# Optimization experiments

Hardware: AMD Instinct MI355X
Metric: run time of the kernel (lower is better)

## Reference

```python
import jax, jax.numpy as jnp
import numpy as np

L_F, D_F = 32, 16      # fast window / hop
L_S, D_S = 32, 16      # slow window / hop
H = 32                 # SSM hidden dim
GH = 64                # GRU hidden dim
N_GRU = 4


def setup_inputs() -> dict:
    key = jax.random.key(0)
    ks = jax.random.split(key, 16)
    B, T = 2, 64000
    s = 0.1
    return {
        "x": jax.random.normal(ks[0], (B, T), jnp.float32),
        # slow branch input FC (1 -> GH), stored as (in, out)
        "slow_in_W": jax.random.normal(ks[1], (1, GH), jnp.float32) * s,
        "slow_in_b": jax.random.normal(ks[2], (GH,), jnp.float32) * s,
        # 4 stacked GRU layers, torch gate order [r, z, n], stored (in, 3*GH)
        "gru_Wih": jax.random.normal(ks[3], (N_GRU, GH, 3 * GH), jnp.float32) * s,
        "gru_Whh": jax.random.normal(ks[4], (N_GRU, GH, 3 * GH), jnp.float32) * s,
        "gru_bih": jax.random.normal(ks[5], (N_GRU, 3 * GH), jnp.float32) * s,
        "gru_bhh": jax.random.normal(ks[6], (N_GRU, 3 * GH), jnp.float32) * s,
        # slow branch output FC (GH -> GH)
        "slow_out_W": jax.random.normal(ks[7], (GH, GH), jnp.float32) * s,
        "slow_out_b": jax.random.normal(ks[8], (GH,), jnp.float32) * s,
        # slow_to_ssm (GH -> 2H)
        "s2s_W": jax.random.normal(ks[9], (GH, 2 * H), jnp.float32) * s,
        "s2s_b": jax.random.normal(ks[10], (2 * H,), jnp.float32) * s,
        # fast branch F_IN (1 -> H) and F_OUT (H -> 1)
        "fin_W": jax.random.normal(ks[11], (1, H), jnp.float32) * s,
        "fin_b": jax.random.normal(ks[12], (H,), jnp.float32) * s,
        "fout_W": jax.random.normal(ks[13], (H, 1), jnp.float32) * s,
        "fout_b": jax.random.normal(ks[14], (1,), jnp.float32) * s,
    }


def _forward(x, slow_in_W, slow_in_b, gru_Wih, gru_Whh, gru_bih, gru_bhh,
             slow_out_W, slow_out_b, s2s_W, s2s_b, fin_W, fin_b, fout_W, fout_b):
    B, T = x.shape
    nf = (T - L_F) // D_F + 1   # fast frame count
    ns = (T - L_S) // D_S + 1   # slow frame count
    fidx = jnp.arange(nf)[:, None] * D_F + jnp.arange(L_F)[None, :]  # (nf, L_F)
    sidx = jnp.arange(ns)[:, None] * D_S + jnp.arange(L_S)[None, :]  # (ns, L_S)
    frames = x[:, fidx]                                  # (B, nf, L_F)  == x.unfold

    BS = B * ns
    xs = x[:, sidx].reshape(BS, L_S, 1)
    h = jax.nn.relu(xs @ slow_in_W + slow_in_b)          # (BS, L_S, GH)
    for l in range(N_GRU):
        Whh, bhh = gru_Whh[l], gru_bhh[l]
        xg = h @ gru_Wih[l] + gru_bih[l]                 # (BS, L_S, 3GH)

        def step(hc, xg_t, Whh=Whh, bhh=bhh):
            hg = hc @ Whh + bhh
            r = jax.nn.sigmoid(xg_t[:, :GH] + hg[:, :GH])
            z = jax.nn.sigmoid(xg_t[:, GH:2 * GH] + hg[:, GH:2 * GH])
            n = jnp.tanh(xg_t[:, 2 * GH:] + r * hg[:, 2 * GH:])
            hn = (1.0 - z) * n + z * hc
            return hn, hn

        _, seq = jax.lax.scan(step, jnp.zeros((BS, GH), x.dtype), jnp.swapaxes(xg, 0, 1))
        h = jax.nn.relu(jnp.swapaxes(seq, 0, 1))         # (BS, L_S, GH)
    slow_feat = h[:, -1, :] @ slow_out_W + slow_out_b    # (BS, GH)

    # ---- modulation parameters ----
    eps = (slow_feat @ s2s_W + s2s_b).reshape(B, ns, 2 * H)
    A_s = jax.nn.sigmoid(eps[..., :H])                   # (B, ns, H)
    g_s = eps[..., H:]
    delta = D_S // D_F
    A_flat = jnp.repeat(A_s, delta, axis=1)[:, :nf].reshape(B * nf, H)
    g_flat = jnp.repeat(g_s, delta, axis=1)[:, :nf].reshape(B * nf, H)

    # ---- fast branch: diagonal SSM h_t = A*h_{t-1} + g * F_IN(x_t) ----
    ff = frames.reshape(B * nf, L_F, 1)
    x_emb = (ff @ fin_W + fin_b) * g_flat[:, None, :]    # (B*nf, L_F, H)

    def ssm_step(hc, xt):
        hn = A_flat * hc + xt
        return hn, hn

    _, hall = jax.lax.scan(ssm_step, jnp.zeros((B * nf, H), x.dtype),
                           jnp.swapaxes(x_emb, 0, 1))
    hall = jnp.swapaxes(hall, 0, 1)                      # (B*nf, L_F, H)
    s_hat = (hall @ fout_W + fout_b)[..., 0].reshape(B, nf, L_F)

    # ---- overlap-add (F.fold) ----
    out = jnp.zeros((B, T), x.dtype).at[:, fidx].add(s_hat)
    return out


def reference(x, slow_in_W, slow_in_b, gru_Wih, gru_Whh, gru_bih, gru_bhh,
              slow_out_W, slow_out_b, s2s_W, s2s_b, fin_W, fin_b, fout_W, fout_b):
    return _forward(x, slow_in_W, slow_in_b, gru_Wih, gru_Whh, gru_bih, gru_bhh,
                    slow_out_W, slow_out_b, s2s_W, s2s_b, fin_W, fin_b, fout_W, fout_b)
```

## Files before the change

kernel.cpp:

```cpp
#include <hip/hip_runtime.h>

#define GH 64
#define LS 32
#define HF 32
#define DS 16

#define NLOG2E -1.4426950408889634f
#define P2LOG2E 2.8853900817779268f

typedef short bf16x8 __attribute__((ext_vector_type(8)));
typedef float f32x4 __attribute__((ext_vector_type(4)));

#define MFMA16(a, b, c) __builtin_amdgcn_mfma_f32_16x16x32_bf16(a, b, c, 0, 0, 0)

__device__ __forceinline__ unsigned int f2bf_rne(float f) {
    unsigned int u = __float_as_uint(f);
    return (u + 0x7FFFu + ((u >> 16) & 1u)) >> 16;
}
__device__ __forceinline__ unsigned short f2bf_h(float f) {
    return (unsigned short)((__float_as_uint(f) + 0x8000u) >> 16);
}
__device__ __forceinline__ unsigned int pack_trunc(float v0, float v1) {
    return __builtin_amdgcn_perm(__float_as_uint(v1), __float_as_uint(v0),
                                 0x07060302u);
}
__device__ __forceinline__ bf16x8 as_frag(uint4 u) {
    union { uint4 a; bf16x8 b; } cv; cv.a = u; return cv.b;
}

__device__ __forceinline__ bf16x8 ld_afrag(const unsigned short* slot, int m,
                                           int quad, int half) {
    int b   = half * 4 + quad;
    int idx = (m << 6) + ((b ^ (m & 7)) << 3);
    return as_frag(*reinterpret_cast<const uint4*>(slot + idx));
}

__global__ __launch_bounds__(256) void prep_weights(
    const float* __restrict__ Wih, const float* __restrict__ Whh,
    const float* __restrict__ soW, const float* __restrict__ s2sW,
    unsigned short* __restrict__ wsW,
    float* __restrict__ out, int out_n)
{
    int gid = blockIdx.x * 256 + threadIdx.x;
    int nthreads = gridDim.x * 256;

    {
        float4* out4 = reinterpret_cast<float4*>(out);
        int n4 = out_n >> 2;
        for (int i = gid; i < n4; i += nthreads)
            out4[i] = make_float4(0.f, 0.f, 0.f, 0.f);
        int tail = out_n & 3;
        if (gid < tail) out[n4 * 4 + gid] = 0.0f;
    }

    if (gid >= 104 * 1024) return;

    float v;
    int dest;
    if (gid < 98304) {
        int g     = gid % 192;
        int r1    = gid / 192;
        int k     = r1 & 63;
        int r2    = r1 >> 6;
        int l     = r2 & 3;
        int which = r2 >> 2;
        int m3  = g / 64;
        int col = g - m3 * 64;
        const float* W = which ? Whh : Wih;
        v = W[(size_t)l * GH * 192 + k * 192 + g];
        v *= (m3 == 2) ? P2LOG2E : NLOG2E;
        int jt = col >> 4, c = col & 15;
        int mat  = which * 3 + m3;
        int rest = (l * 6 + mat) * 4 + jt;
        int kc = k >> 5, j = k & 7, lane = ((k >> 3) & 3) * 16 + c;
        dest = rest * 1024 + kc * 512 + lane * 8 + j;
    } else {
        int e   = gid - 98304;
        int col = e & 63;
        int k   = (e >> 6) & 63;
        int m2  = e >> 12;
        v = (m2 ? s2sW : soW)[k * 64 + col];
        if (m2 && col < 32) v *= NLOG2E;
        int jt = col >> 4, c = col & 15;
        int rest = 96 + m2 * 4 + jt;
        int kc = k >> 5, j = k & 7, lane = ((k >> 3) & 3) * 16 + c;
        dest = rest * 1024 + kc * 512 + lane * 8 + j;
    }
    wsW[dest] = (unsigned short)f2bf_rne(v);
}

__global__ __launch_bounds__(1024, 4) void slowfast_fused(
    const float* __restrict__ x,
    const float* __restrict__ siW,  const float* __restrict__ sib,
    const float* __restrict__ bih,  const float* __restrict__ bhh,
    const float* __restrict__ sob,  const float* __restrict__ s2sb,
    const float* __restrict__ finW, const float* __restrict__ finb,
    const float* __restrict__ foutW, const float* __restrict__ foutb,
    const unsigned short* __restrict__ wsW,
    float* __restrict__ out,
    int T, int ns, int BS)
{
    __shared__ __align__(16) unsigned short bnd[3 * 2 * 1024];
    __shared__ __align__(16) unsigned short hrec[4 * 2 * 1024];
    __shared__ __align__(16) unsigned short hfin[1024];
    __shared__ float xs[16 * 33];
    __shared__ float AG[16 * 65];
    __shared__ __align__(16) float swS[64], sbS[64];

    const int tid  = threadIdx.x;
    const int lane = tid & 63;
    const int w    = tid >> 6;
    const int l    = w >> 2;
    const int jt   = w & 3;
    const int c    = lane & 15;
    const int quad = lane >> 4;
    const int col  = jt * 16 + c;
    const int seqbase = blockIdx.x * 16;
    const uint4* wf = reinterpret_cast<const uint4*>(wsW);

    if (tid < 512) {
        int seq = tid >> 5, t = tid & 31;
        int q = seqbase + seq; if (q > BS - 1) q = BS - 1;
        int b  = (q >= ns) ? 1 : 0;
        int si = q - b * ns;
        xs[seq * 33 + t] = x[b * T + si * DS + t];
    } else if (tid < 576) {
        int i = tid - 512;
        swS[i] = siW[i];
        sbS[i] = sib[i];
    }

    bf16x8 BiR[2], BiZ[2], BiN[2], BhR[2], BhZ[2], BhN[2];
    #pragma unroll
    for (int kc = 0; kc < 2; ++kc) {
        int base = (l * 24 + jt) * 128 + kc * 64 + lane;
        BiR[kc] = as_frag(wf[base]);
        BiZ[kc] = as_frag(wf[base + 512]);
        BiN[kc] = as_frag(wf[base + 1024]);
        BhR[kc] = as_frag(wf[base + 1536]);
        BhZ[kc] = as_frag(wf[base + 2048]);
        BhN[kc] = as_frag(wf[base + 2560]);
    }
    float bRs  = NLOG2E  * (bih[l * 192 + col]      + bhh[l * 192 + col]);
    float bZs  = NLOG2E  * (bih[l * 192 + 64 + col] + bhh[l * 192 + 64 + col]);
    float bNIs = P2LOG2E * bih[l * 192 + 128 + col];
    float bNHs = P2LOG2E * bhh[l * 192 + 128 + col];
    const f32x4 vbR  = (f32x4){bRs,  bRs,  bRs,  bRs};
    const f32x4 vbZ  = (f32x4){bZs,  bZs,  bZs,  bZs};
    const f32x4 vbNI = (f32x4){bNIs, bNIs, bNIs, bNIs};
    const f32x4 vbNH = (f32x4){bNHs, bNHs, bNHs, bNHs};

    int wIdx[4];
    #pragma unroll
    for (int i = 0; i < 4; ++i) {
        int row = quad * 4 + i;
        wIdx[i] = (row << 6) + ((((col >> 3) ^ (row & 7))) << 3) + (col & 7);
    }

    float hprev[4] = {0.0f, 0.0f, 0.0f, 0.0f};
    const float4* sw4 = reinterpret_cast<const float4*>(swS);
    const float4* sb4 = reinterpret_cast<const float4*>(sbS);

    #pragma unroll 1
    for (int tau = 0; tau < 35; ++tau) {
        __syncthreads();
        int t = tau - l;
        if (t < 0 || t >= 32) continue;

        bf16x8 a0, a1;
        if (l == 0) {
            float xv = xs[c * 33 + t];
            float4 wA = sw4[quad * 2],     wB = sw4[quad * 2 + 1];
            float4 bA = sb4[quad * 2],     bB = sb4[quad * 2 + 1];
            float4 wC = sw4[8 + quad * 2], wD = sw4[8 + quad * 2 + 1];
            float4 bC = sb4[8 + quad * 2], bD = sb4[8 + quad * 2 + 1];
            uint4 u;
            u.x = pack_trunc(fmaxf(fmaf(xv, wA.x, bA.x), 0.f),
                             fmaxf(fmaf(xv, wA.y, bA.y), 0.f));
            u.y = pack_trunc(fmaxf(fmaf(xv, wA.z, bA.z), 0.f),
                             fmaxf(fmaf(xv, wA.w, bA.w), 0.f));
            u.z = pack_trunc(fmaxf(fmaf(xv, wB.x, bB.x), 0.f),
                             fmaxf(fmaf(xv, wB.y, bB.y), 0.f));
            u.w = pack_trunc(fmaxf(fmaf(xv, wB.z, bB.z), 0.f),
                             fmaxf(fmaf(xv, wB.w, bB.w), 0.f));
            a0 = as_frag(u);
            u.x = pack_trunc(fmaxf(fmaf(xv, wC.x, bC.x), 0.f),
                             fmaxf(fmaf(xv, wC.y, bC.y), 0.f));
            u.y = pack_trunc(fmaxf(fmaf(xv, wC.z, bC.z), 0.f),
                             fmaxf(fmaf(xv, wC.w, bC.w), 0.f));
            u.z = pack_trunc(fmaxf(fmaf(xv, wD.x, bD.x), 0.f),
                             fmaxf(fmaf(xv, wD.y, bD.y), 0.f));
            u.w = pack_trunc(fmaxf(fmaf(xv, wD.z, bD.z), 0.f),
                             fmaxf(fmaf(xv, wD.w, bD.w), 0.f));
            a1 = as_frag(u);
        } else {
            const unsigned short* src = bnd + (((l - 1) << 1) + (t & 1)) * 1024;
            a0 = ld_afrag(src, c, quad, 0);
            a1 = ld_afrag(src, c, quad, 1);
        }

        f32x4 aR  = MFMA16(a0, BiR[0], vbR);
        f32x4 aZ  = MFMA16(a0, BiZ[0], vbZ);
        f32x4 aNI = MFMA16(a0, BiN[0], vbNI);
        aR  = MFMA16(a1, BiR[1], aR);
        aZ  = MFMA16(a1, BiZ[1], aZ);
        aNI = MFMA16(a1, BiN[1], aNI);
        f32x4 aNH = vbNH;
        if (t > 0) {
            const unsigned short* hb = hrec + ((l << 1) + ((t - 1) & 1)) * 1024;
            bf16x8 h0 = ld_afrag(hb, c, quad, 0);
            bf16x8 h1 = ld_afrag(hb, c, quad, 1);
            aR  = MFMA16(h0, BhR[0], aR);
            aZ  = MFMA16(h0, BhZ[0], aZ);
            aNH = MFMA16(h0, BhN[0], aNH);
            aR  = MFMA16(h1, BhR[1], aR);
            aZ  = MFMA16(h1, BhZ[1], aZ);
            aNH = MFMA16(h1, BhN[1], aNH);
        }
        unsigned short* wr = hrec + ((l << 1) + (t & 1)) * 1024;
        unsigned short* wb = (l < 3) ? (bnd + ((l << 1) + (t & 1)) * 1024)
                                     : hfin;
        #pragma unroll
        for (int i = 0; i < 4; ++i) {
            float r  = __builtin_amdgcn_rcpf(1.0f + __builtin_amdgcn_exp2f(aR[i]));
            float z  = __builtin_amdgcn_rcpf(1.0f + __builtin_amdgcn_exp2f(aZ[i]));
            float e  = __builtin_amdgcn_exp2f(fmaf(r, aNH[i], aNI[i]));
            float n  = fmaf(-2.0f, __builtin_amdgcn_rcpf(e + 1.0f), 1.0f);
            float hn = fmaf(z, hprev[i] - n, n);
            hprev[i] = hn;
            wr[wIdx[i]] = f2bf_h(hn);
            wb[wIdx[i]] = f2bf_h(fmaxf(hn, 0.0f));
        }
    }
    __syncthreads();

    f32x4 accS;
    bf16x8 Bso[2], Bs2[2];
    if (w < 4) {
        bf16x8 e0 = ld_afrag(hfin, c, quad, 0);
        bf16x8 e1 = ld_afrag(hfin, c, quad, 1);
        #pragma unroll
        for (int kc = 0; kc < 2; ++kc) {
            Bso[kc] = as_frag(wf[(96 + jt)  * 128 + kc * 64 + lane]);
            Bs2[kc] = as_frag(wf[(100 + jt) * 128 + kc * 64 + lane]);
        }
        float sb = sob[col];
        accS = (f32x4){sb, sb, sb, sb};
        accS = MFMA16(e0, Bso[0], accS);
        accS = MFMA16(e1, Bso[1], accS);
    }
    __syncthreads();
    if (w < 4) {
        #pragma unroll
        for (int i = 0; i < 4; ++i)
            hfin[wIdx[i]] = f2bf_h(accS[i]);
    }
    __syncthreads();
    if (w < 4) {
        bf16x8 s0 = ld_afrag(hfin, c, quad, 0);
        bf16x8 s1 = ld_afrag(hfin, c, quad, 1);
        float eb = (jt < 2) ? NLOG2E * s2sb[col] : s2sb[col];
        f32x4 accE = (f32x4){eb, eb, eb, eb};
        accE = MFMA16(s0, Bs2[0], accE);
        accE = MFMA16(s1, Bs2[1], accE);
        #pragma unroll
        for (int i = 0; i < 4; ++i) {
            int row = quad * 4 + i;
            float v = accE[i];
            AG[row * 65 + col] = (jt < 2)
                ? __builtin_amdgcn_rcpf(1.0f + __builtin_amdgcn_exp2f(v)) : v;
        }
    }
    __syncthreads();
    if (tid < 512) {
        int fch   = tid & 31;
        int frame = tid >> 5;
        int q = seqbase + frame;
        if (q < BS) {
            float Gfw = finW[fch], Gbw = finb[fch];
            float cFo = foutW[fch], cfb = foutb[0];
            int b  = (q >= ns) ? 1 : 0;
            int fi = q - b * ns;
            float cA = AG[frame * 65 + fch];
            float cG = AG[frame * 65 + 32 + fch];
            float Gf = Gfw * cG;
            float Gb = Gbw * cG;
            float h = 0.0f;
            const float* xrow = xs + frame * 33;
            float* op = out + (size_t)b * T + fi * DS;
            #pragma unroll 1
            for (int t = 0; t < LS; ++t) {
                h = fmaf(cA, h, fmaf(xrow[t], Gf, Gb));
                float s = h * cFo;
                s += __shfl_xor(s, 1);
                s += __shfl_xor(s, 2);
                s += __shfl_xor(s, 4);
                s += __shfl_xor(s, 8);
                s += __shfl_xor(s, 16);
                if (fch == 0) atomicAdd(&op[t], s + cfb);
            }
        }
    }
}

extern "C" void kernel_launch(void* const* d_in, const int* in_sizes, int n_in,
                              void* d_out, int out_size, void* d_ws, size_t ws_size,
                              hipStream_t stream)
{
    (void)n_in; (void)ws_size;
    const float* x     = (const float*)d_in[0];
    const float* siW   = (const float*)d_in[1];
    const float* sib   = (const float*)d_in[2];
    const float* Wih   = (const float*)d_in[3];
    const float* Whh   = (const float*)d_in[4];
    const float* bih   = (const float*)d_in[5];
    const float* bhh   = (const float*)d_in[6];
    const float* soW   = (const float*)d_in[7];
    const float* sob   = (const float*)d_in[8];
    const float* s2sW  = (const float*)d_in[9];
    const float* s2sb  = (const float*)d_in[10];
    const float* finW  = (const float*)d_in[11];
    const float* finb  = (const float*)d_in[12];
    const float* foutW = (const float*)d_in[13];
    const float* foutb = (const float*)d_in[14];

    int T  = in_sizes[0] / 2;
    int ns = (T - LS) / DS + 1;
    int BS = 2 * ns;
    int nblocks = (BS + 15) / 16;

    unsigned short* wsW = (unsigned short*)d_ws;

    prep_weights<<<dim3(416), dim3(256), 0, stream>>>(
        Wih, Whh, soW, s2sW, wsW, (float*)d_out, out_size);

    slowfast_fused<<<dim3(nblocks), dim3(1024), 0, stream>>>(
        x, siW, sib, bih, bhh, sob, s2sb, finW, finb, foutW, foutb,
        wsW, (float*)d_out, T, ns, BS);
}
```

Before: 179.3 us.

## Halve block size so each wave computes two GRU column tiles

The fused kernel now launches 512 threads per block instead of 1024. Each wave handles two 16-column output tiles of its GRU layer, sharing the A-fragment loads across both tiles and doubling its MFMA work per step. This cuts redundant LDS reads of the input and hidden fragments and reduces how many waves meet at each barrier. In exchange, each wave holds twice as many weight fragments in registers, which may lower occupancy and lengthen each wave's serial dependency chain.

```diff
diff --git a/kernel.cpp b/kernel.cpp
--- a/kernel.cpp
+++ b/kernel.cpp
@@ -89,7 +89,25 @@
     wsW[dest] = (unsigned short)f2bf_rne(v);
 }
 
-__global__ __launch_bounds__(1024, 4) void slowfast_fused(
+__device__ __forceinline__ void gate4(const f32x4& aR, const f32x4& aZ,
+                                      const f32x4& aNI, const f32x4& aNH,
+                                      float* hprev, unsigned short* wr,
+                                      unsigned short* wb, const int* wIdx)
+{
+    #pragma unroll
+    for (int i = 0; i < 4; ++i) {
+        float r  = __builtin_amdgcn_rcpf(1.0f + __builtin_amdgcn_exp2f(aR[i]));
+        float z  = __builtin_amdgcn_rcpf(1.0f + __builtin_amdgcn_exp2f(aZ[i]));
+        float e  = __builtin_amdgcn_exp2f(fmaf(r, aNH[i], aNI[i]));
+        float n  = fmaf(-2.0f, __builtin_amdgcn_rcpf(e + 1.0f), 1.0f);
+        float hn = fmaf(z, hprev[i] - n, n);
+        hprev[i] = hn;
+        wr[wIdx[i]] = f2bf_h(hn);
+        wb[wIdx[i]] = f2bf_h(fmaxf(hn, 0.0f));
+    }
+}
+
+__global__ __launch_bounds__(512, 2) void slowfast_fused(
     const float* __restrict__ x,
     const float* __restrict__ siW,  const float* __restrict__ sib,
     const float* __restrict__ bih,  const float* __restrict__ bhh,
@@ -110,54 +128,63 @@
     const int tid  = threadIdx.x;
     const int lane = tid & 63;
     const int w    = tid >> 6;
-    const int l    = w >> 2;
-    const int jt   = w & 3;
+    const int l    = w >> 1;
+    const int hg   = w & 1;
     const int c    = lane & 15;
     const int quad = lane >> 4;
-    const int col  = jt * 16 + c;
     const int seqbase = blockIdx.x * 16;
     const uint4* wf = reinterpret_cast<const uint4*>(wsW);
 
-    if (tid < 512) {
+    {
         int seq = tid >> 5, t = tid & 31;
         int q = seqbase + seq; if (q > BS - 1) q = BS - 1;
         int b  = (q >= ns) ? 1 : 0;
         int si = q - b * ns;
         xs[seq * 33 + t] = x[b * T + si * DS + t];
-    } else if (tid < 576) {
-        int i = tid - 512;
-        swS[i] = siW[i];
-        sbS[i] = sib[i];
-    }
-
-    bf16x8 BiR[2], BiZ[2], BiN[2], BhR[2], BhZ[2], BhN[2];
+    }
+    if (tid < 64) { swS[tid] = siW[tid]; sbS[tid] = sib[tid]; }
+
+    bf16x8 BiR[2][2], BiZ[2][2], BiN[2][2], BhR[2][2], BhZ[2][2], BhN[2][2];
     #pragma unroll
-    for (int kc = 0; kc < 2; ++kc) {
-        int base = (l * 24 + jt) * 128 + kc * 64 + lane;
-        BiR[kc] = as_frag(wf[base]);
-        BiZ[kc] = as_frag(wf[base + 512]);
-        BiN[kc] = as_frag(wf[base + 1024]);
-        BhR[kc] = as_frag(wf[base + 1536]);
-        BhZ[kc] = as_frag(wf[base + 2048]);
-        BhN[kc] = as_frag(wf[base + 2560]);
-    }
-    float bRs  = NLOG2E  * (bih[l * 192 + col]      + bhh[l * 192 + col]);
-    float bZs  = NLOG2E  * (bih[l * 192 + 64 + col] + bhh[l * 192 + 64 + col]);
-    float bNIs = P2LOG2E * bih[l * 192 + 128 + col];
-    float bNHs = P2LOG2E * bhh[l * 192 + 128 + col];
-    const f32x4 vbR  = (f32x4){bRs,  bRs,  bRs,  bRs};
-    const f32x4 vbZ  = (f32x4){bZs,  bZs,  bZs,  bZs};
-    const f32x4 vbNI = (f32x4){bNIs, bNIs, bNIs, bNIs};
-    const f32x4 vbNH = (f32x4){bNHs, bNHs, bNHs, bNHs};
-
-    int wIdx[4];
+    for (int g = 0; g < 2; ++g) {
+        int jt2 = hg * 2 + g;
+        #pragma unroll
+        for (int kc = 0; kc < 2; ++kc) {
+            int base = (l * 24 + jt2) * 128 + kc * 64 + lane;
+            BiR[g][kc] = as_frag(wf[base]);
+            BiZ[g][kc] = as_frag(wf[base + 512]);
+            BiN[g][kc] = as_frag(wf[base + 1024]);
+            BhR[g][kc] = as_frag(wf[base + 1536]);
+            BhZ[g][kc] = as_frag(wf[base + 2048]);
+            BhN[g][kc] = as_frag(wf[base + 2560]);
+        }
+    }
+    f32x4 vbR[2], vbZ[2], vbNI[2], vbNH[2];
     #pragma unroll
-    for (int i = 0; i < 4; ++i) {
-        int row = quad * 4 + i;
-        wIdx[i] = (row << 6) + ((((col >> 3) ^ (row & 7))) << 3) + (col & 7);
-    }
-
-    float hprev[4] = {0.0f, 0.0f, 0.0f, 0.0f};
+    for (int g = 0; g < 2; ++g) {
+        int col2 = (hg * 2 + g) * 16 + c;
+        float bRs  = NLOG2E  * (bih[l * 192 + col2]      + bhh[l * 192 + col2]);
+        float bZs  = NLOG2E  * (bih[l * 192 + 64 + col2] + bhh[l * 192 + 64 + col2]);
+        float bNIs = P2LOG2E * bih[l * 192 + 128 + col2];
+        float bNHs = P2LOG2E * bhh[l * 192 + 128 + col2];
+        vbR[g]  = (f32x4){bRs,  bRs,  bRs,  bRs};
+        vbZ[g]  = (f32x4){bZs,  bZs,  bZs,  bZs};
+        vbNI[g] = (f32x4){bNIs, bNIs, bNIs, bNIs};
+        vbNH[g] = (f32x4){bNHs, bNHs, bNHs, bNHs};
+    }
+
+    int wIdxG[2][4];
+    #pragma unroll
+    for (int g = 0; g < 2; ++g) {
+        int colg = (hg * 2 + g) * 16 + c;
+        #pragma unroll
+        for (int i = 0; i < 4; ++i) {
+            int row = quad * 4 + i;
+            wIdxG[g][i] = (row << 6) + ((((colg >> 3) ^ (row & 7))) << 3) + (colg & 7);
+        }
+    }
+
+    float hprev[2][4] = {{0.f,0.f,0.f,0.f},{0.f,0.f,0.f,0.f}};
     const float4* sw4 = reinterpret_cast<const float4*>(swS);
     const float4* sb4 = reinterpret_cast<const float4*>(sbS);
 
@@ -199,44 +226,50 @@
             a1 = ld_afrag(src, c, quad, 1);
         }
 
-        f32x4 aR  = MFMA16(a0, BiR[0], vbR);
-        f32x4 aZ  = MFMA16(a0, BiZ[0], vbZ);
-        f32x4 aNI = MFMA16(a0, BiN[0], vbNI);
-        aR  = MFMA16(a1, BiR[1], aR);
-        aZ  = MFMA16(a1, BiZ[1], aZ);
-        aNI = MFMA16(a1, BiN[1], aNI);
-        f32x4 aNH = vbNH;
+        f32x4 aR[2], aZ[2], aNI[2], aNH[2];
+        #pragma unroll
+        for (int g = 0; g < 2; ++g) {
+            aR[g]  = MFMA16(a0, BiR[g][0], vbR[g]);
+            aZ[g]  = MFMA16(a0, BiZ[g][0], vbZ[g]);
+            aNI[g] = MFMA16(a0, BiN[g][0], vbNI[g]);
+            aR[g]  = MFMA16(a1, BiR[g][1], aR[g]);
+            aZ[g]  = MFMA16(a1, BiZ[g][1], aZ[g]);
+            aNI[g] = MFMA16(a1, BiN[g][1], aNI[g]);
+            aNH[g] = vbNH[g];
+        }
         if (t > 0) {
             const unsigned short* hb = hrec + ((l << 1) + ((t - 1) & 1)) * 1024;
             bf16x8 h0 = ld_afrag(hb, c, quad, 0);
             bf16x8 h1 = ld_afrag(hb, c, quad, 1);
-            aR  = MFMA16(h0, BhR[0], aR);
-            aZ  = MFMA16(h0, BhZ[0], aZ);
-            aNH = MFMA16(h0, BhN[0], aNH);
-            aR  = MFMA16(h1, BhR[1], aR);
-            aZ  = MFMA16(h1, BhZ[1], aZ);
-            aNH = MFMA16(h1, BhN[1], aNH);
+            #pragma unroll
+            for (int g = 0; g < 2; ++g) {
+                aR[g]  = MFMA16(h0, BhR[g][0], aR[g]);
+                aZ[g]  = MFMA16(h0, BhZ[g][0], aZ[g]);
+                aNH[g] = MFMA16(h0, BhN[g][0], aNH[g]);
+                aR[g]  = MFMA16(h1, BhR[g][1], aR[g]);
+                aZ[g]  = MFMA16(h1, BhZ[g][1], aZ[g]);
+                aNH[g] = MFMA16(h1, BhN[g][1], aNH[g]);
+            }
         }
         unsigned short* wr = hrec + ((l << 1) + (t & 1)) * 1024;
         unsigned short* wb = (l < 3) ? (bnd + ((l << 1) + (t & 1)) * 1024)
                                      : hfin;
-        #pragma unroll
-        for (int i = 0; i < 4; ++i) {
-            float r  = __builtin_amdgcn_rcpf(1.0f + __builtin_amdgcn_exp2f(aR[i]));
-            float z  = __builtin_amdgcn_rcpf(1.0f + __builtin_amdgcn_exp2f(aZ[i]));
-            float e  = __builtin_amdgcn_exp2f(fmaf(r, aNH[i], aNI[i]));
-            float n  = fmaf(-2.0f, __builtin_amdgcn_rcpf(e + 1.0f), 1.0f);
-            float hn = fmaf(z, hprev[i] - n, n);
-            hprev[i] = hn;
-            wr[wIdx[i]] = f2bf_h(hn);
-            wb[wIdx[i]] = f2bf_h(fmaxf(hn, 0.0f));
-        }
+        gate4(aR[0], aZ[0], aNI[0], aNH[0], hprev[0], wr, wb, wIdxG[0]);
+        gate4(aR[1], aZ[1], aNI[1], aNH[1], hprev[1], wr, wb, wIdxG[1]);
     }
     __syncthreads();
 
     f32x4 accS;
     bf16x8 Bso[2], Bs2[2];
+    int wIdxE[4];
+    const int jt = w;
+    const int colE = jt * 16 + c;
     if (w < 4) {
+        #pragma unroll
+        for (int i = 0; i < 4; ++i) {
+            int row = quad * 4 + i;
+            wIdxE[i] = (row << 6) + ((((colE >> 3) ^ (row & 7))) << 3) + (colE & 7);
+        }
         bf16x8 e0 = ld_afrag(hfin, c, quad, 0);
         bf16x8 e1 = ld_afrag(hfin, c, quad, 1);
         #pragma unroll
@@ -244,7 +277,7 @@
             Bso[kc] = as_frag(wf[(96 + jt)  * 128 + kc * 64 + lane]);
             Bs2[kc] = as_frag(wf[(100 + jt) * 128 + kc * 64 + lane]);
         }
-        float sb = sob[col];
+        float sb = sob[colE];
         accS = (f32x4){sb, sb, sb, sb};
         accS = MFMA16(e0, Bso[0], accS);
         accS = MFMA16(e1, Bso[1], accS);
@@ -253,13 +286,13 @@
     if (w < 4) {
         #pragma unroll
         for (int i = 0; i < 4; ++i)
-            hfin[wIdx[i]] = f2bf_h(accS[i]);
+            hfin[wIdxE[i]] = f2bf_h(accS[i]);
     }
     __syncthreads();
     if (w < 4) {
         bf16x8 s0 = ld_afrag(hfin, c, quad, 0);
         bf16x8 s1 = ld_afrag(hfin, c, quad, 1);
-        float eb = (jt < 2) ? NLOG2E * s2sb[col] : s2sb[col];
+        float eb = (jt < 2) ? NLOG2E * s2sb[colE] : s2sb[colE];
         f32x4 accE = (f32x4){eb, eb, eb, eb};
         accE = MFMA16(s0, Bs2[0], accE);
         accE = MFMA16(s1, Bs2[1], accE);
@@ -267,37 +300,39 @@
         for (int i = 0; i < 4; ++i) {
             int row = quad * 4 + i;
             float v = accE[i];
-            AG[row * 65 + col] = (jt < 2)
+            AG[row * 65 + colE] = (jt < 2)
                 ? __builtin_amdgcn_rcpf(1.0f + __builtin_amdgcn_exp2f(v)) : v;
         }
     }
     __syncthreads();
-    if (tid < 512) {
+    {
         int fch   = tid & 31;
         int frame = tid >> 5;
-        int q = seqbase + frame;
-        if (q < BS) {
-            float Gfw = finW[fch], Gbw = finb[fch];
-            float cFo = foutW[fch], cfb = foutb[0];
-            int b  = (q >= ns) ? 1 : 0;
-            int fi = q - b * ns;
-            float cA = AG[frame * 65 + fch];
-            float cG = AG[frame * 65 + 32 + fch];
-            float Gf = Gfw * cG;
-            float Gb = Gbw * cG;
-            float h = 0.0f;
-            const float* xrow = xs + frame * 33;
-            float* op = out + (size_t)b * T + fi * DS;
-            #pragma unroll 1
-            for (int t = 0; t < LS; ++t) {
-                h = fmaf(cA, h, fmaf(xrow[t], Gf, Gb));
-                float s = h * cFo;
-                s += __shfl_xor(s, 1);
-                s += __shfl_xor(s, 2);
-                s += __shfl_xor(s, 4);
-                s += __shfl_xor(s, 8);
-                s += __shfl_xor(s, 16);
-                if (fch == 0) atomicAdd(&op[t], s + cfb);
+        if (frame < 16) {
+            int q = seqbase + frame;
+            if (q < BS) {
+                float Gfw = finW[fch], Gbw = finb[fch];
+                float cFo = foutW[fch], cfb = foutb[0];
+                int b  = (q >= ns) ? 1 : 0;
+                int fi = q - b * ns;
+                float cA = AG[frame * 65 + fch];
+                float cG = AG[frame * 65 + 32 + fch];
+                float Gf = Gfw * cG;
+                float Gb = Gbw * cG;
+                float h = 0.0f;
+                const float* xrow = xs + frame * 33;
+                float* op = out + (size_t)b * T + fi * DS;
+                #pragma unroll 1
+                for (int t = 0; t < LS; ++t) {
+                    h = fmaf(cA, h, fmaf(xrow[t], Gf, Gb));
+                    float s = h * cFo;
+                    s += __shfl_xor(s, 1);
+                    s += __shfl_xor(s, 2);
+                    s += __shfl_xor(s, 4);
+                    s += __shfl_xor(s, 8);
+                    s += __shfl_xor(s, 16);
+                    if (fch == 0) atomicAdd(&op[t], s + cfb);
+                }
             }
         }
     }
@@ -334,7 +369,7 @@
     prep_weights<<<dim3(416), dim3(256), 0, stream>>>(
         Wih, Whh, soW, s2sW, wsW, (float*)d_out, out_size);
 
-    slowfast_fused<<<dim3(nblocks), dim3(1024), 0, stream>>>(
+    slowfast_fused<<<dim3(nblocks), dim3(512), 0, stream>>>(
         x, siW, sib, bih, bhh, sob, s2sb, finW, finb, foutW, foutb,
         wsW, (float*)d_out, T, ns, BS);
 }
```

Measured after the change: 181.2 us. No clear change (+1.0%).
